# Kernel optimization log

Measured on AMD Instinct MI355X. Metric: run time of the kernel, lower is better.

## Reference

```python
import jax, jax.numpy as jnp
import numpy as np

V, E, HD, C, B, T = 30000, 256, 512, 9, 128, 256
H = HD // 2  # per-direction hidden size


def setup_inputs() -> dict:
    key = jax.random.key(0)
    ks = iter(jax.random.split(key, 64))

    def rn(shape, scale):
        return jax.random.normal(next(ks), shape, jnp.float32) * scale

    s = 1.0 / np.sqrt(H)
    inp = {}
    inp["x"] = jax.random.randint(next(ks), (B, T), 0, V, dtype=jnp.int32)
    inp["tags"] = jax.random.randint(next(ks), (B, T), 0, C, dtype=jnp.int32)
    inp["mask"] = jnp.ones((B, T), dtype=bool)
    inp["emb"] = rn((V, E), 1.0)
    in_dims = [E, HD]
    for l in range(2):
        for d in ("f", "b"):
            inp[f"w_ih_l{l}{d}"] = rn((4 * H, in_dims[l]), s)
            inp[f"w_hh_l{l}{d}"] = rn((4 * H, H), s)
            inp[f"b_ih_l{l}{d}"] = rn((4 * H,), s)
            inp[f"b_hh_l{l}{d}"] = rn((4 * H,), s)
    inp["lin_w"] = rn((C, HD), 1.0 / np.sqrt(HD))
    inp["lin_b"] = rn((C,), 0.01)
    inp["trans"] = rn((C, C), 0.1)
    inp["start"] = rn((C,), 0.1)
    inp["end"] = rn((C,), 0.1)
    return inp


def _lstm_dir(x, w_ih, w_hh, b_ih, b_hh):
    # x: [T, B, in]; PyTorch gate order i, f, g, o
    Bn = x.shape[1]
    Hn = w_hh.shape[1]

    def step(carry, xt):
        h, c = carry
        g = xt @ w_ih.T + b_ih + h @ w_hh.T + b_hh
        i, f, gg, o = jnp.split(g, 4, axis=-1)
        c = jax.nn.sigmoid(f) * c + jax.nn.sigmoid(i) * jnp.tanh(gg)
        h = jax.nn.sigmoid(o) * jnp.tanh(c)
        return (h, c), h

    z = jnp.zeros((Bn, Hn), x.dtype)
    _, hs = jax.lax.scan(step, (z, z), x)
    return hs  # [T, B, H]


def _bilstm(x, pf, pb):
    hf = _lstm_dir(x, *pf)
    hb = _lstm_dir(x[::-1], *pb)[::-1]
    return jnp.concatenate([hf, hb], axis=-1)  # [T, B, 2H]


def _crf_nll(em, tags, mask, trans, start, end):
    # em: [T, B, C] (time-major emissions); tags, mask: [B, T]
    tags_t = tags.T              # [T, B]
    mf = mask.astype(em.dtype).T  # [T, B]
    Bn = tags.shape[0]
    bidx = jnp.arange(Bn)
    # numerator: score of the gold path
    num = start[tags_t[0]] + em[0, bidx, tags_t[0]]
    step_em = jnp.take_along_axis(em[1:], tags_t[1:, :, None], axis=2)[..., 0]  # [T-1, B]
    step_sc = trans[tags_t[:-1], tags_t[1:]] + step_em
    num = num + (step_sc * mf[1:]).sum(0)
    lengths = mask.sum(1).astype(jnp.int32)
    last_tags = tags[bidx, lengths - 1]
    num = num + end[last_tags]
    # denominator: forward algorithm (logsumexp scan over time)
    alpha0 = start + em[0]  # [B, C]

    def step(alpha, inp):
        e, m = inp
        nxt = jax.nn.logsumexp(alpha[:, :, None] + trans[None] + e[:, None, :], axis=1)
        return jnp.where(m[:, None] > 0, nxt, alpha), None

    alpha, _ = jax.lax.scan(step, alpha0, (em[1:], mf[1:]))
    logZ = jax.nn.logsumexp(alpha + end, axis=1)
    return -(num - logZ).mean()


def reference(x, tags, mask, emb,
              w_ih_l0f, w_hh_l0f, b_ih_l0f, b_hh_l0f,
              w_ih_l0b, w_hh_l0b, b_ih_l0b, b_hh_l0b,
              w_ih_l1f, w_hh_l1f, b_ih_l1f, b_hh_l1f,
              w_ih_l1b, w_hh_l1b, b_ih_l1b, b_hh_l1b,
              lin_w, lin_b, trans, start, end):
    xt = emb[x].transpose(1, 0, 2)  # [T, B, E]
    h1 = _bilstm(xt, (w_ih_l0f, w_hh_l0f, b_ih_l0f, b_hh_l0f),
                 (w_ih_l0b, w_hh_l0b, b_ih_l0b, b_hh_l0b))
    h2 = _bilstm(h1, (w_ih_l1f, w_hh_l1f, b_ih_l1f, b_hh_l1f),
                 (w_ih_l1b, w_hh_l1b, b_ih_l1b, b_hh_l1b))
    em = h2 @ lin_w.T + lin_b  # [T, B, C]
    return _crf_nll(em, tags, mask, trans, start, end)
```

## Files before the change

kernel.cpp:

```cpp
#include <hip/hip_runtime.h>

#define T_LEN 256
#define B_SZ  128
#define E_DIM 256
#define NC    9

typedef short bf16x8 __attribute__((ext_vector_type(8)));
typedef float f32x4  __attribute__((ext_vector_type(4)));
typedef int   i32x4  __attribute__((ext_vector_type(4)));
typedef unsigned short u16x4 __attribute__((ext_vector_type(4)));
typedef unsigned int   u32x2 __attribute__((ext_vector_type(2)));

__device__ __forceinline__ float bf2f(unsigned short u) {
    return __uint_as_float(((unsigned)u) << 16);
}
__device__ __forceinline__ unsigned short f2bf(float f) {
    unsigned x = __float_as_uint(f);
    unsigned r = x + 0x7FFFu + ((x >> 16) & 1u);
    return (unsigned short)(r >> 16);
}
__device__ __forceinline__ float rcpf(float x) { return __builtin_amdgcn_rcpf(x); }
__device__ __forceinline__ float sigf(float x) { return rcpf(1.0f + __expf(-x)); }
__device__ __forceinline__ float tanh_fast(float x) {
    float e = __expf(2.0f * x);
    return 1.0f - 2.0f * rcpf(e + 1.0f);
}

__global__ void k_prep(const float* __restrict__ i0f, const float* __restrict__ i0b,
                       const float* __restrict__ i1f, const float* __restrict__ i1b,
                       unsigned short* __restrict__ d0f, unsigned short* __restrict__ d0b,
                       unsigned short* __restrict__ d1f, unsigned short* __restrict__ d1b) {
    int j = blockIdx.y;
    int idx = blockIdx.x * 256 + threadIdx.x;
    int n = (j < 2) ? 262144 : 524288;
    if (idx < n) {
        const float* s = (j == 0) ? i0f : (j == 1) ? i0b : (j == 2) ? i1f : i1b;
        unsigned short* d = (j == 0) ? d0f : (j == 1) ? d0b : (j == 2) ? d1f : d1b;
        d[idx] = f2bf(s[idx]);
    }
}

__global__ __launch_bounds__(256) void k_packq(
    const float* __restrict__ h0, const float* __restrict__ h1,
    const float* __restrict__ h2, const float* __restrict__ h3,
    unsigned* __restrict__ q0, unsigned* __restrict__ q1,
    unsigned* __restrict__ q2, unsigned* __restrict__ q3,
    float* __restrict__ s0, float* __restrict__ s1,
    float* __restrict__ s2, float* __restrict__ s3) {
    int bx = blockIdx.x;
    int mat = bx >> 6, grp = bx & 63;
    int w = grp >> 2, g = grp & 3;
    const float* src = (mat == 0) ? h0 : (mat == 1) ? h1 : (mat == 2) ? h2 : h3;
    unsigned* dst    = (mat == 0) ? q0 : (mat == 1) ? q1 : (mat == 2) ? q2 : q3;
    float* Sv        = (mat == 0) ? s0 : (mat == 1) ? s1 : (mat == 2) ? s2 : s3;

    int tid = threadIdx.x;
    int rr = tid >> 4, ks = (tid & 15) * 16;
    const float* rp = src + (size_t)(g * 256 + w * 16 + rr) * 256 + ks;
    float v[16];
    float mx = 0.f;
#pragma unroll
    for (int j = 0; j < 16; j++) { v[j] = rp[j]; mx = fmaxf(mx, fabsf(v[j])); }
    __shared__ float red[256];
    red[tid] = mx;
    __syncthreads();
    for (int s = 128; s > 0; s >>= 1) {
        if (tid < s) red[tid] = fmaxf(red[tid], red[tid + s]);
        __syncthreads();
    }
    float bmax = red[0];
    float inv = bmax > 1e-30f ? 127.f / bmax : 0.f;
    if (tid == 0) Sv[w * 4 + g] = bmax > 1e-30f ? bmax * (1.f / 16129.f) : 0.f;
    int p = w * 64 + g * 16 + rr;
#pragma unroll
    for (int j4 = 0; j4 < 4; j4++) {
        unsigned pk = 0;
#pragma unroll
        for (int b = 0; b < 4; b++) {
            int q = __float2int_rn(v[j4 * 4 + b] * inv);
            pk |= ((unsigned)(q & 255)) << (8 * b);
        }
        dst[(size_t)p * 64 + (tid & 15) * 4 + j4] = pk;
    }
}

__global__ void k_bias4(const float* __restrict__ a0, const float* __restrict__ b0,
                        const float* __restrict__ a1, const float* __restrict__ b1,
                        const float* __restrict__ a2, const float* __restrict__ b2,
                        const float* __restrict__ a3, const float* __restrict__ b3,
                        float* __restrict__ d) {
    int idx = blockIdx.x * 256 + threadIdx.x;
    if (idx < 4096) {
        int j = idx >> 10, i = idx & 1023;
        const float* a = (j == 0) ? a0 : (j == 1) ? a1 : (j == 2) ? a2 : a3;
        const float* b = (j == 0) ? b0 : (j == 1) ? b1 : (j == 2) ? b2 : b3;
        d[idx] = a[i] + b[i];
    }
}

__global__ void k_embed(const int* __restrict__ x, const float* __restrict__ emb,
                        unsigned short* __restrict__ X0) {
    int row = blockIdx.x * 4 + (threadIdx.x >> 6);
    int lane = threadIdx.x & 63;
    int t = row >> 7, b = row & 127;
    int xi = x[b * T_LEN + t];
    const float4 e = *reinterpret_cast<const float4*>(emb + (size_t)xi * E_DIM + lane * 4);
    ushort4 o;
    o.x = f2bf(e.x); o.y = f2bf(e.y); o.z = f2bf(e.z); o.w = f2bf(e.w);
    *reinterpret_cast<ushort4*>(X0 + (size_t)row * E_DIM + lane * 4) = o;
}

template<int K>
__global__ __launch_bounds__(256, 1) void k_gemm2(const unsigned short* __restrict__ A,
                                                  const unsigned short* __restrict__ W,
                                                  const float* __restrict__ bias,
                                                  unsigned short* __restrict__ out) {
    int m0 = blockIdx.x * 128;
    int w = threadIdx.x >> 6, l = threadIdx.x & 63;
    int lr = l & 15, hi = l >> 4;
    bf16x8 af[2][K / 32];
#pragma unroll
    for (int s = 0; s < 2; s++)
#pragma unroll
        for (int kk = 0; kk < K / 32; kk++)
            af[s][kk] = *reinterpret_cast<const bf16x8*>(
                A + (size_t)(m0 + w * 32 + s * 16 + lr) * K + kk * 32 + hi * 8);
#pragma unroll 1
    for (int tn = 0; tn < 16; tn++) {
        int n0 = tn * 64;
        f32x4 acc[4][2];
        f32x4 z = {0.f, 0.f, 0.f, 0.f};
#pragma unroll
        for (int c = 0; c < 4; c++) { acc[c][0] = z; acc[c][1] = z; }
#pragma unroll
        for (int kk = 0; kk < K / 32; kk++) {
#pragma unroll
            for (int c = 0; c < 4; c++) {
                bf16x8 wf = *reinterpret_cast<const bf16x8*>(
                    W + (size_t)(n0 + c * 16 + lr) * K + kk * 32 + hi * 8);
                acc[c][0] = __builtin_amdgcn_mfma_f32_16x16x32_bf16(wf, af[0][kk], acc[c][0], 0, 0, 0);
                acc[c][1] = __builtin_amdgcn_mfma_f32_16x16x32_bf16(wf, af[1][kk], acc[c][1], 0, 0, 0);
            }
        }
#pragma unroll
        for (int c = 0; c < 4; c++) {
            float4 bv = *reinterpret_cast<const float4*>(bias + n0 + c * 16 + hi * 4);
#pragma unroll
            for (int s = 0; s < 2; s++) {
                unsigned short hb[4];
                hb[0] = f2bf(acc[c][s][0] + bv.x);
                hb[1] = f2bf(acc[c][s][1] + bv.y);
                hb[2] = f2bf(acc[c][s][2] + bv.z);
                hb[3] = f2bf(acc[c][s][3] + bv.w);
                u32x2 dv;
                dv[0] = (unsigned)hb[0] | ((unsigned)hb[1] << 16);
                dv[1] = (unsigned)hb[2] | ((unsigned)hb[3] << 16);
                *reinterpret_cast<u32x2*>(out + (size_t)(m0 + w * 32 + s * 16 + lr) * 1024
                                          + n0 + c * 16 + hi * 4) = dv;
            }
        }
    }
}

__global__ __launch_bounds__(1024, 1) void k_lstm9(const unsigned short* __restrict__ Gf,
                                                   const unsigned short* __restrict__ Gb,
                                                   const unsigned* __restrict__ Wqf,
                                                   const unsigned* __restrict__ Wqb,
                                                   const float* __restrict__ Sf,
                                                   const float* __restrict__ Sb,
                                                   unsigned short* __restrict__ Hout) {
    __shared__ char smem[73728];
    unsigned short* gbuf = (unsigned short*)smem;
    char* hqb = smem + 65536;

    int bx = blockIdx.x;
    int dir = bx >> 3, rg = bx & 7;
    const unsigned short* G = dir ? Gb : Gf;
    const unsigned* Wq = dir ? Wqb : Wqf;
    const float* S = dir ? Sb : Sf;

    int tid = threadIdx.x;
    int w = tid >> 6, l = tid & 63;
    int lr = l & 15, hi = l >> 4;

    float sw[4];
#pragma unroll
    for (int g = 0; g < 4; g++) sw[g] = S[w * 4 + g];

    long wq[4][8];
    {
        const unsigned* wb = Wq + (size_t)(w * 64 + lr) * 64 + hi * 2;
#pragma unroll
        for (int g = 0; g < 4; g++)
#pragma unroll
            for (int kk = 0; kk < 8; kk++)
                wq[g][kk] = *reinterpret_cast<const long*>(wb + g * 1024 + kk * 8);
    }

    int off0 = tid * 16, off1 = 16384 + tid * 16;
    int r0 = off0 >> 11, in0 = off0 & 2047;
    int r1 = off1 >> 11, in1 = off1 & 2047;
    int gsrc0 = (rg * 16 + r0) * 1024 + ((in0 ^ ((r0 & 7) << 4)) >> 1);
    int gsrc1 = (rg * 16 + r1) * 1024 + ((in1 ^ ((r1 & 7) << 4)) >> 1);
    int Xs = (lr & 7) << 4, Xh = lr << 4;
    int gro[4];
#pragma unroll
    for (int g = 0; g < 4; g++) gro[g] = lr * 2048 + ((g * 512 + w * 32 + hi * 8) ^ Xs);
    int hwo = lr * 256 + ((w * 16 + hi * 4) ^ Xh);

    int t0 = dir ? (T_LEN - 1) : 0;
    long dg = dir ? -(long)(B_SZ * 1024) : (long)(B_SZ * 1024);
    long dh = dir ? -(long)(B_SZ * 512)  : (long)(B_SZ * 512);
    const unsigned short* G0 = G + (size_t)t0 * (B_SZ * 1024);
    const unsigned short* Gpre = G0 + dg;
    unsigned short* hst = Hout + ((size_t)t0 * B_SZ + rg * 16 + lr) * 512
                          + dir * 256 + w * 16 + hi * 4;

    *reinterpret_cast<int2*>(hqb + tid * 8) = make_int2(0, 0);
    __builtin_amdgcn_global_load_lds(
        (const __attribute__((address_space(1))) unsigned int*)(G0 + gsrc0),
        (__attribute__((address_space(3))) unsigned int*)(gbuf + w * 512), 16, 0, 0);
    __builtin_amdgcn_global_load_lds(
        (const __attribute__((address_space(1))) unsigned int*)(G0 + gsrc1),
        (__attribute__((address_space(3))) unsigned int*)(gbuf + 8192 + w * 512), 16, 0, 0);
    __syncthreads();

    float c4[4] = {0.f, 0.f, 0.f, 0.f};
    i32x4 z4 = {0, 0, 0, 0};

    for (int s = 0; s < T_LEN; ++s) {
        int rdg = (s & 1) * 16384;
        int rdh = (s & 1) * 4096;

        if (s < T_LEN - 1) {
            unsigned short* dst = gbuf + (16384 - rdg);
            __builtin_amdgcn_global_load_lds(
                (const __attribute__((address_space(1))) unsigned int*)(Gpre + gsrc0),
                (__attribute__((address_space(3))) unsigned int*)(dst + w * 512), 16, 0, 0);
            __builtin_amdgcn_global_load_lds(
                (const __attribute__((address_space(1))) unsigned int*)(Gpre + gsrc1),
                (__attribute__((address_space(3))) unsigned int*)(dst + 8192 + w * 512), 16, 0, 0);
            Gpre += dg;
        }

        char* hrb = hqb + rdh;
        i32x4 acc[4];
#pragma unroll
        for (int g = 0; g < 4; g++) acc[g] = z4;
#pragma unroll
        for (int kk = 0; kk < 8; kk++) {
            long hf = *reinterpret_cast<const long*>(hrb + lr * 256 + ((kk * 32 + hi * 8) ^ Xh));
#pragma unroll
            for (int g = 0; g < 4; g++)
                acc[g] = __builtin_amdgcn_mfma_i32_16x16x32_i8(wq[g][kk], hf, acc[g], 0, 0, 0);
        }

        char* grb = (char*)(gbuf + rdg);
        u16x4 g4[4];
#pragma unroll
        for (int g = 0; g < 4; g++)
            g4[g] = *reinterpret_cast<const u16x4*>(grb + gro[g]);
        unsigned short hb[4];
        unsigned hqw = 0;
#pragma unroll
        for (int r = 0; r < 4; r++) {
            float xi = (float)acc[0][r] * sw[0] + bf2f(g4[0][r]);
            float xf = (float)acc[1][r] * sw[1] + bf2f(g4[1][r]);
            float xg = (float)acc[2][r] * sw[2] + bf2f(g4[2][r]);
            float xo = (float)acc[3][r] * sw[3] + bf2f(g4[3][r]);
            float cv = sigf(xf) * c4[r] + sigf(xi) * tanh_fast(xg);
            c4[r] = cv;
            float hv = sigf(xo) * tanh_fast(cv);
            hb[r] = f2bf(hv);
            int q = __float2int_rn(hv * 127.f);
            hqw |= ((unsigned)(q & 255)) << (8 * r);
        }

        *reinterpret_cast<unsigned*>(hqb + (4096 - rdh) + hwo) = hqw;
        u32x2 dv;
        dv[0] = (unsigned)hb[0] | ((unsigned)hb[1] << 16);
        dv[1] = (unsigned)hb[2] | ((unsigned)hb[3] << 16);
        *reinterpret_cast<u32x2*>(hst) = dv;
        hst += dh;

        __syncthreads();
    }
}

__global__ __launch_bounds__(256) void k_emis(const unsigned short* __restrict__ H2,
                                              const float* __restrict__ lw,
                                              const float* __restrict__ lb,
                                              float* __restrict__ EM) {
    int row = blockIdx.x * 4 + (threadIdx.x >> 6);
    int lane = threadIdx.x & 63;
    bf16x8 hv = *reinterpret_cast<const bf16x8*>(H2 + (size_t)row * 512 + lane * 8);
    float hf[8];
#pragma unroll
    for (int j = 0; j < 8; j++) hf[j] = bf2f((unsigned short)hv[j]);
#pragma unroll
    for (int cc = 0; cc < NC; cc++) {
        const float* wr = lw + cc * 512 + lane * 8;
        float4 w0 = *reinterpret_cast<const float4*>(wr);
        float4 w1 = *reinterpret_cast<const float4*>(wr + 4);
        float d = hf[0] * w0.x + hf[1] * w0.y + hf[2] * w0.z + hf[3] * w0.w +
                  hf[4] * w1.x + hf[5] * w1.y + hf[6] * w1.z + hf[7] * w1.w;
#pragma unroll
        for (int off = 32; off >= 1; off >>= 1) d += __shfl_down(d, off, 64);
        if (lane == 0) EM[(size_t)row * NC + cc] = d + lb[cc];
    }
}

__global__ __launch_bounds__(64) void k_crf(const float* __restrict__ EM,
                                            const int* __restrict__ tags,
                                            const float* __restrict__ trans,
                                            const float* __restrict__ start,
                                            const float* __restrict__ end,
                                            float* __restrict__ partials) {
    int b = blockIdx.x, tid = threadIdx.x;
    __shared__ float tr[160];
    for (int i = tid; i < 160; i += 64) tr[i] = (i < 81) ? trans[i] : 0.f;
    __syncthreads();

    int j = tid;
    float alpha = -1e30f;
    if (j < 9) alpha = start[j] + EM[b * NC + j];

    for (int t = 1; t < T_LEN; t++) {
        float av[9];
#pragma unroll
        for (int i = 0; i < 9; i++) av[i] = __shfl(alpha, i, 64) + tr[i * 9 + j];
        float m = av[0];
#pragma unroll
        for (int i = 1; i < 9; i++) m = fmaxf(m, av[i]);
        float sum = 0.f;
#pragma unroll
        for (int i = 0; i < 9; i++) sum += expf(av[i] - m);
        float e = (j < 9) ? EM[(size_t)t * (B_SZ * NC) + b * NC + j] : 0.f;
        float na = m + logf(sum) + e;
        alpha = (j < 9) ? na : -1e30f;
    }
    float aend[9];
    float m2 = -1e30f;
#pragma unroll
    for (int i = 0; i < 9; i++) {
        aend[i] = __shfl(alpha, i, 64) + end[i];
        m2 = fmaxf(m2, aend[i]);
    }
    float s2 = 0.f;
#pragma unroll
    for (int i = 0; i < 9; i++) s2 += expf(aend[i] - m2);
    float logZ = m2 + logf(s2);

    float nsum = 0.f;
    for (int t = 1 + tid; t < T_LEN; t += 64) {
        int tp = tags[b * T_LEN + t - 1], tc = tags[b * T_LEN + t];
        nsum += tr[tp * 9 + tc] + EM[(size_t)t * (B_SZ * NC) + b * NC + tc];
    }
#pragma unroll
    for (int off = 32; off >= 1; off >>= 1) nsum += __shfl_down(nsum, off, 64);

    if (tid == 0) {
        int t0 = tags[b * T_LEN], tl = tags[b * T_LEN + T_LEN - 1];
        float num = start[t0] + EM[b * NC + t0] + nsum + end[tl];
        partials[b] = num - logZ;
    }
}

__global__ void k_reduce(const float* __restrict__ partials, float* __restrict__ out) {
    int tid = threadIdx.x;
    float v = partials[tid];
#pragma unroll
    for (int off = 32; off >= 1; off >>= 1) v += __shfl_down(v, off, 64);
    __shared__ float sm[2];
    if ((tid & 63) == 0) sm[tid >> 6] = v;
    __syncthreads();
    if (tid == 0) out[0] = -(sm[0] + sm[1]) / 128.0f;
}

extern "C" void kernel_launch(void* const* d_in, const int* in_sizes, int n_in,
                              void* d_out, int out_size, void* d_ws, size_t ws_size,
                              hipStream_t stream) {
    const int*   x     = (const int*)d_in[0];
    const int*   tags  = (const int*)d_in[1];
    const float* emb   = (const float*)d_in[3];
    const float* w_ih[4] = {(const float*)d_in[4],  (const float*)d_in[8],
                            (const float*)d_in[12], (const float*)d_in[16]};
    const float* w_hh[4] = {(const float*)d_in[5],  (const float*)d_in[9],
                            (const float*)d_in[13], (const float*)d_in[17]};
    const float* b_ih[4] = {(const float*)d_in[6],  (const float*)d_in[10],
                            (const float*)d_in[14], (const float*)d_in[18]};
    const float* b_hh[4] = {(const float*)d_in[7],  (const float*)d_in[11],
                            (const float*)d_in[15], (const float*)d_in[19]};
    const float* lin_w = (const float*)d_in[20];
    const float* lin_b = (const float*)d_in[21];
    const float* trans = (const float*)d_in[22];
    const float* start = (const float*)d_in[23];
    const float* endv  = (const float*)d_in[24];

    char* ws = (char*)d_ws;
    size_t off = 0;
    auto alloc = [&](size_t bytes) -> void* {
        size_t a = (off + 255) & ~(size_t)255;
        off = a + bytes;
        return (void*)(ws + a);
    };

    unsigned short* wb_ih0f = (unsigned short*)alloc(1024 * 256 * 2);
    unsigned short* wb_ih0b = (unsigned short*)alloc(1024 * 256 * 2);
    unsigned short* wb_ih1f = (unsigned short*)alloc(1024 * 512 * 2);
    unsigned short* wb_ih1b = (unsigned short*)alloc(1024 * 512 * 2);
    unsigned* wq0f = (unsigned*)alloc(1024 * 256);
    unsigned* wq0b = (unsigned*)alloc(1024 * 256);
    unsigned* wq1f = (unsigned*)alloc(1024 * 256);
    unsigned* wq1b = (unsigned*)alloc(1024 * 256);
    float* sq0f = (float*)alloc(64 * 4);
    float* sq0b = (float*)alloc(64 * 4);
    float* sq1f = (float*)alloc(64 * 4);
    float* sq1b = (float*)alloc(64 * 4);
    float* bsum = (float*)alloc(4096 * 4);
    unsigned short* X0 = (unsigned short*)alloc((size_t)32768 * 256 * 2);
    unsigned short* Gf = (unsigned short*)alloc((size_t)32768 * 1024 * 2);
    unsigned short* Gb = (unsigned short*)alloc((size_t)32768 * 1024 * 2);
    unsigned short* H1 = (unsigned short*)alloc((size_t)32768 * 512 * 2);
    unsigned short* H2 = (unsigned short*)alloc((size_t)32768 * 512 * 2);
    float* EM = (float*)alloc((size_t)32768 * NC * 4);
    float* partials = (float*)alloc(128 * 4);

    hipLaunchKernelGGL(k_prep, dim3(2048, 4), dim3(256), 0, stream,
                       w_ih[0], w_ih[1], w_ih[2], w_ih[3],
                       wb_ih0f, wb_ih0b, wb_ih1f, wb_ih1b);
    hipLaunchKernelGGL(k_packq, dim3(256), dim3(256), 0, stream,
                       w_hh[0], w_hh[1], w_hh[2], w_hh[3],
                       wq0f, wq0b, wq1f, wq1b,
                       sq0f, sq0b, sq1f, sq1b);
    hipLaunchKernelGGL(k_bias4, dim3(16), dim3(256), 0, stream,
                       b_ih[0], b_hh[0], b_ih[1], b_hh[1],
                       b_ih[2], b_hh[2], b_ih[3], b_hh[3], bsum);

    hipLaunchKernelGGL(k_embed, dim3(8192), dim3(256), 0, stream, x, emb, X0);

    hipLaunchKernelGGL(k_gemm2<256>, dim3(256), dim3(256), 0, stream, X0, wb_ih0f, bsum, Gf);
    hipLaunchKernelGGL(k_gemm2<256>, dim3(256), dim3(256), 0, stream, X0, wb_ih0b, bsum + 1024, Gb);
    hipLaunchKernelGGL(k_lstm9, dim3(16), dim3(1024), 0, stream,
                       Gf, Gb, wq0f, wq0b, sq0f, sq0b, H1);

    hipLaunchKernelGGL(k_gemm2<512>, dim3(256), dim3(256), 0, stream, H1, wb_ih1f, bsum + 2048, Gf);
    hipLaunchKernelGGL(k_gemm2<512>, dim3(256), dim3(256), 0, stream, H1, wb_ih1b, bsum + 3072, Gb);
    hipLaunchKernelGGL(k_lstm9, dim3(16), dim3(1024), 0, stream,
                       Gf, Gb, wq1f, wq1b, sq1f, sq1b, H2);

    hipLaunchKernelGGL(k_emis, dim3(8192), dim3(256), 0, stream, H2, lin_w, lin_b, EM);
    hipLaunchKernelGGL(k_crf, dim3(128), dim3(64), 0, stream, EM, tags, trans, start, endv, partials);
    hipLaunchKernelGGL(k_reduce, dim3(1), dim3(128), 0, stream, partials, (float*)d_out);
}
```

Measured before the change: 1.801 ms.

## Merge gate GEMMs, pre-scale gates by log2e, interleave gate layout, batch-major emissions

The forward and backward input-projection GEMMs are merged into one launch, with the N range split across grid z so the grid holds more blocks. Gate preactivations, biases and recurrent scales are pre-multiplied by log2(e), so the LSTM cell can use exp2 directly, and sigmoid*tanh products are fused into a single reciprocal each. The gate columns are also interleaved so each lane reads its four gates with two 16-byte LDS loads, and h is packed to bf16 with a packed convert instruction. Emissions are stored batch-major so the CRF reads are contiguous. Clamping the exp2 arguments and merging reciprocals changes numerics slightly.

Result: slower. 1.908 ms (+5.9%).

```diff
diff --git a/kernel.cpp b/kernel.cpp
--- a/kernel.cpp
+++ b/kernel.cpp
@@ -8,8 +8,10 @@
 typedef short bf16x8 __attribute__((ext_vector_type(8)));
 typedef float f32x4  __attribute__((ext_vector_type(4)));
 typedef int   i32x4  __attribute__((ext_vector_type(4)));
-typedef unsigned short u16x4 __attribute__((ext_vector_type(4)));
+typedef unsigned short u16x8 __attribute__((ext_vector_type(8)));
 typedef unsigned int   u32x2 __attribute__((ext_vector_type(2)));
+
+#define L2E 1.4426950408889634f
 
 __device__ __forceinline__ float bf2f(unsigned short u) {
     return __uint_as_float(((unsigned)u) << 16);
@@ -20,11 +22,7 @@
     return (unsigned short)(r >> 16);
 }
 __device__ __forceinline__ float rcpf(float x) { return __builtin_amdgcn_rcpf(x); }
-__device__ __forceinline__ float sigf(float x) { return rcpf(1.0f + __expf(-x)); }
-__device__ __forceinline__ float tanh_fast(float x) {
-    float e = __expf(2.0f * x);
-    return 1.0f - 2.0f * rcpf(e + 1.0f);
-}
+__device__ __forceinline__ float ex2(float x) { return __builtin_amdgcn_exp2f(x); }
 
 __global__ void k_prep(const float* __restrict__ i0f, const float* __restrict__ i0b,
                        const float* __restrict__ i1f, const float* __restrict__ i1b,
@@ -70,7 +68,7 @@
     }
     float bmax = red[0];
     float inv = bmax > 1e-30f ? 127.f / bmax : 0.f;
-    if (tid == 0) Sv[w * 4 + g] = bmax > 1e-30f ? bmax * (1.f / 16129.f) : 0.f;
+    if (tid == 0) Sv[w * 4 + g] = bmax > 1e-30f ? bmax * (L2E / 16129.f) : 0.f;
     int p = w * 64 + g * 16 + rr;
 #pragma unroll
     for (int j4 = 0; j4 < 4; j4++) {
@@ -94,7 +92,7 @@
         int j = idx >> 10, i = idx & 1023;
         const float* a = (j == 0) ? a0 : (j == 1) ? a1 : (j == 2) ? a2 : a3;
         const float* b = (j == 0) ? b0 : (j == 1) ? b1 : (j == 2) ? b2 : b3;
-        d[idx] = a[i] + b[i];
+        d[idx] = (a[i] + b[i]) * L2E;
     }
 }
 
@@ -111,10 +109,16 @@
 }
 
 template<int K>
-__global__ __launch_bounds__(256, 1) void k_gemm2(const unsigned short* __restrict__ A,
-                                                  const unsigned short* __restrict__ W,
-                                                  const float* __restrict__ bias,
-                                                  unsigned short* __restrict__ out) {
+__global__ __launch_bounds__(256, 1) void k_gemm3(const unsigned short* __restrict__ A,
+                                                  const unsigned short* __restrict__ Wf,
+                                                  const unsigned short* __restrict__ Wb,
+                                                  const float* __restrict__ biasf,
+                                                  const float* __restrict__ biasb,
+                                                  unsigned short* __restrict__ outf,
+                                                  unsigned short* __restrict__ outb) {
+    const unsigned short* W = blockIdx.y ? Wb : Wf;
+    const float* bias = blockIdx.y ? biasb : biasf;
+    unsigned short* out = blockIdx.y ? outb : outf;
     int m0 = blockIdx.x * 128;
     int w = threadIdx.x >> 6, l = threadIdx.x & 63;
     int lr = l & 15, hi = l >> 4;
@@ -126,7 +130,7 @@
             af[s][kk] = *reinterpret_cast<const bf16x8*>(
                 A + (size_t)(m0 + w * 32 + s * 16 + lr) * K + kk * 32 + hi * 8);
 #pragma unroll 1
-    for (int tn = 0; tn < 16; tn++) {
+    for (int tn = blockIdx.z * 8; tn < (int)blockIdx.z * 8 + 8; tn++) {
         int n0 = tn * 64;
         f32x4 acc[4][2];
         f32x4 z = {0.f, 0.f, 0.f, 0.f};
@@ -144,31 +148,33 @@
         }
 #pragma unroll
         for (int c = 0; c < 4; c++) {
-            float4 bv = *reinterpret_cast<const float4*>(bias + n0 + c * 16 + hi * 4);
+            int corig = n0 + c * 16 + hi * 4;
+            float4 bv = *reinterpret_cast<const float4*>(bias + corig);
+            int col2 = ((corig & 255) >> 2) * 16 + (corig >> 8) * 4;
 #pragma unroll
             for (int s = 0; s < 2; s++) {
                 unsigned short hb[4];
-                hb[0] = f2bf(acc[c][s][0] + bv.x);
-                hb[1] = f2bf(acc[c][s][1] + bv.y);
-                hb[2] = f2bf(acc[c][s][2] + bv.z);
-                hb[3] = f2bf(acc[c][s][3] + bv.w);
+                hb[0] = f2bf(fmaf(acc[c][s][0], L2E, bv.x));
+                hb[1] = f2bf(fmaf(acc[c][s][1], L2E, bv.y));
+                hb[2] = f2bf(fmaf(acc[c][s][2], L2E, bv.z));
+                hb[3] = f2bf(fmaf(acc[c][s][3], L2E, bv.w));
                 u32x2 dv;
                 dv[0] = (unsigned)hb[0] | ((unsigned)hb[1] << 16);
                 dv[1] = (unsigned)hb[2] | ((unsigned)hb[3] << 16);
                 *reinterpret_cast<u32x2*>(out + (size_t)(m0 + w * 32 + s * 16 + lr) * 1024
-                                          + n0 + c * 16 + hi * 4) = dv;
+                                          + col2) = dv;
             }
         }
     }
 }
 
-__global__ __launch_bounds__(1024, 1) void k_lstm9(const unsigned short* __restrict__ Gf,
-                                                   const unsigned short* __restrict__ Gb,
-                                                   const unsigned* __restrict__ Wqf,
-                                                   const unsigned* __restrict__ Wqb,
-                                                   const float* __restrict__ Sf,
-                                                   const float* __restrict__ Sb,
-                                                   unsigned short* __restrict__ Hout) {
+__global__ __launch_bounds__(1024, 1) void k_lstm10(const unsigned short* __restrict__ Gf,
+                                                    const unsigned short* __restrict__ Gb,
+                                                    const unsigned* __restrict__ Wqf,
+                                                    const unsigned* __restrict__ Wqb,
+                                                    const float* __restrict__ Sf,
+                                                    const float* __restrict__ Sb,
+                                                    unsigned short* __restrict__ Hout) {
     __shared__ char smem[73728];
     unsigned short* gbuf = (unsigned short*)smem;
     char* hqb = smem + 65536;
@@ -203,9 +209,10 @@
     int gsrc0 = (rg * 16 + r0) * 1024 + ((in0 ^ ((r0 & 7) << 4)) >> 1);
     int gsrc1 = (rg * 16 + r1) * 1024 + ((in1 ^ ((r1 & 7) << 4)) >> 1);
     int Xs = (lr & 7) << 4, Xh = lr << 4;
-    int gro[4];
-#pragma unroll
-    for (int g = 0; g < 4; g++) gro[g] = lr * 2048 + ((g * 512 + w * 32 + hi * 8) ^ Xs);
+    int hg32 = (w * 4 + hi) * 32;
+    int gro2[2];
+    gro2[0] = lr * 2048 + (hg32 ^ Xs);
+    gro2[1] = lr * 2048 + ((hg32 + 16) ^ Xs);
     int hwo = lr * 256 + ((w * 16 + hi * 4) ^ Xh);
 
     int t0 = dir ? (T_LEN - 1) : 0;
@@ -256,30 +263,34 @@
         }
 
         char* grb = (char*)(gbuf + rdg);
-        u16x4 g4[4];
-#pragma unroll
-        for (int g = 0; g < 4; g++)
-            g4[g] = *reinterpret_cast<const u16x4*>(grb + gro[g]);
-        unsigned short hb[4];
+        u16x8 g01 = *reinterpret_cast<const u16x8*>(grb + gro2[0]);
+        u16x8 g23 = *reinterpret_cast<const u16x8*>(grb + gro2[1]);
         unsigned hqw = 0;
+        float hv4[4];
 #pragma unroll
         for (int r = 0; r < 4; r++) {
-            float xi = (float)acc[0][r] * sw[0] + bf2f(g4[0][r]);
-            float xf = (float)acc[1][r] * sw[1] + bf2f(g4[1][r]);
-            float xg = (float)acc[2][r] * sw[2] + bf2f(g4[2][r]);
-            float xo = (float)acc[3][r] * sw[3] + bf2f(g4[3][r]);
-            float cv = sigf(xf) * c4[r] + sigf(xi) * tanh_fast(xg);
+            float xi = (float)acc[0][r] * sw[0] + bf2f((unsigned short)g01[r]);
+            float xf = (float)acc[1][r] * sw[1] + bf2f((unsigned short)g01[4 + r]);
+            float xg = (float)acc[2][r] * sw[2] + bf2f((unsigned short)g23[r]);
+            float xo = (float)acc[3][r] * sw[3] + bf2f((unsigned short)g23[4 + r]);
+            float sf = rcpf(1.f + ex2(-xf));
+            float a = ex2(-xi);
+            float b = ex2(fminf(xg + xg, 80.f));
+            float p = (b - 1.f) * rcpf((1.f + a) * (1.f + b));
+            float cv = fmaf(sf, c4[r], p);
             c4[r] = cv;
-            float hv = sigf(xo) * tanh_fast(cv);
-            hb[r] = f2bf(hv);
+            float e = ex2(-xo);
+            float d = ex2(fminf(2.8853901f * cv, 80.f));
+            float hv = (d - 1.f) * rcpf((1.f + e) * (1.f + d));
+            hv4[r] = hv;
             int q = __float2int_rn(hv * 127.f);
             hqw |= ((unsigned)(q & 255)) << (8 * r);
         }
 
         *reinterpret_cast<unsigned*>(hqb + (4096 - rdh) + hwo) = hqw;
         u32x2 dv;
-        dv[0] = (unsigned)hb[0] | ((unsigned)hb[1] << 16);
-        dv[1] = (unsigned)hb[2] | ((unsigned)hb[3] << 16);
+        asm("v_cvt_pk_bf16_f32 %0, %1, %2" : "=v"(dv[0]) : "v"(hv4[0]), "v"(hv4[1]));
+        asm("v_cvt_pk_bf16_f32 %0, %1, %2" : "=v"(dv[1]) : "v"(hv4[2]), "v"(hv4[3]));
         *reinterpret_cast<u32x2*>(hst) = dv;
         hst += dh;
 
@@ -293,6 +304,7 @@
                                               float* __restrict__ EM) {
     int row = blockIdx.x * 4 + (threadIdx.x >> 6);
     int lane = threadIdx.x & 63;
+    int t = row >> 7, b = row & 127;
     bf16x8 hv = *reinterpret_cast<const bf16x8*>(H2 + (size_t)row * 512 + lane * 8);
     float hf[8];
 #pragma unroll
@@ -306,7 +318,7 @@
                   hf[4] * w1.x + hf[5] * w1.y + hf[6] * w1.z + hf[7] * w1.w;
 #pragma unroll
         for (int off = 32; off >= 1; off >>= 1) d += __shfl_down(d, off, 64);
-        if (lane == 0) EM[(size_t)row * NC + cc] = d + lb[cc];
+        if (lane == 0) EM[(size_t)b * (T_LEN * NC) + t * NC + cc] = d + lb[cc];
     }
 }
 
@@ -317,13 +329,14 @@
                                             const float* __restrict__ end,
                                             float* __restrict__ partials) {
     int b = blockIdx.x, tid = threadIdx.x;
+    const float* EB = EM + (size_t)b * (T_LEN * NC);
     __shared__ float tr[160];
     for (int i = tid; i < 160; i += 64) tr[i] = (i < 81) ? trans[i] : 0.f;
     __syncthreads();
 
     int j = tid;
     float alpha = -1e30f;
-    if (j < 9) alpha = start[j] + EM[b * NC + j];
+    if (j < 9) alpha = start[j] + EB[j];
 
     for (int t = 1; t < T_LEN; t++) {
         float av[9];
@@ -335,7 +348,7 @@
         float sum = 0.f;
 #pragma unroll
         for (int i = 0; i < 9; i++) sum += expf(av[i] - m);
-        float e = (j < 9) ? EM[(size_t)t * (B_SZ * NC) + b * NC + j] : 0.f;
+        float e = (j < 9) ? EB[t * NC + j] : 0.f;
         float na = m + logf(sum) + e;
         alpha = (j < 9) ? na : -1e30f;
     }
@@ -354,14 +367,14 @@
     float nsum = 0.f;
     for (int t = 1 + tid; t < T_LEN; t += 64) {
         int tp = tags[b * T_LEN + t - 1], tc = tags[b * T_LEN + t];
-        nsum += tr[tp * 9 + tc] + EM[(size_t)t * (B_SZ * NC) + b * NC + tc];
+        nsum += tr[tp * 9 + tc] + EB[t * NC + tc];
     }
 #pragma unroll
     for (int off = 32; off >= 1; off >>= 1) nsum += __shfl_down(nsum, off, 64);
 
     if (tid == 0) {
         int t0 = tags[b * T_LEN], tl = tags[b * T_LEN + T_LEN - 1];
-        float num = start[t0] + EM[b * NC + t0] + nsum + end[tl];
+        float num = start[t0] + EB[t0] + nsum + end[tl];
         partials[b] = num - logZ;
     }
 }
@@ -439,14 +452,14 @@
 
     hipLaunchKernelGGL(k_embed, dim3(8192), dim3(256), 0, stream, x, emb, X0);
 
-    hipLaunchKernelGGL(k_gemm2<256>, dim3(256), dim3(256), 0, stream, X0, wb_ih0f, bsum, Gf);
-    hipLaunchKernelGGL(k_gemm2<256>, dim3(256), dim3(256), 0, stream, X0, wb_ih0b, bsum + 1024, Gb);
-    hipLaunchKernelGGL(k_lstm9, dim3(16), dim3(1024), 0, stream,
+    hipLaunchKernelGGL(k_gemm3<256>, dim3(256, 2, 2), dim3(256), 0, stream,
+                       X0, wb_ih0f, wb_ih0b, bsum, bsum + 1024, Gf, Gb);
+    hipLaunchKernelGGL(k_lstm10, dim3(16), dim3(1024), 0, stream,
                        Gf, Gb, wq0f, wq0b, sq0f, sq0b, H1);
 
-    hipLaunchKernelGGL(k_gemm2<512>, dim3(256), dim3(256), 0, stream, H1, wb_ih1f, bsum + 2048, Gf);
-    hipLaunchKernelGGL(k_gemm2<512>, dim3(256), dim3(256), 0, stream, H1, wb_ih1b, bsum + 3072, Gb);
-    hipLaunchKernelGGL(k_lstm9, dim3(16), dim3(1024), 0, stream,
+    hipLaunchKernelGGL(k_gemm3<512>, dim3(256, 2, 2), dim3(256), 0, stream,
+                       H1, wb_ih1f, wb_ih1b, bsum + 2048, bsum + 3072, Gf, Gb);
+    hipLaunchKernelGGL(k_lstm10, dim3(16), dim3(1024), 0, stream,
                        Gf, Gb, wq1f, wq1b, sq1f, sq1b, H2);
 
     hipLaunchKernelGGL(k_emis, dim3(8192), dim3(256), 0, stream, H2, lin_w, lin_b, EM);
```
